# Performance work log

Measured on AMD Instinct MI355X. Metric: run time of the kernel, lower is better.

## Reference

```python
import jax, jax.numpy as jnp
import numpy as np

B, LD, LQ = 32, 512, 32
E, NF = 300, 4
D = E + NF            # doc_input_size = 304
M = 16                # fofe_max_length == max_len
ALPHA = 0.9
VOCAB = 50000
H = 256
SAMPLE_NUM = 256
POS_N = 128           # int(sample_num * (1 - neg_ratio))
NEG_N = SAMPLE_NUM - POS_N
R = min(M, LD - 2)    # candidate negative lengths = 16
PPL = NEG_N // R + 1  # negatives drawn per length = 9


def setup_inputs() -> dict:
    key = jax.random.key(0)
    ks = jax.random.split(key, 16)
    emb = jax.random.normal(ks[0], (VOCAB, E), jnp.float32) * 0.1
    emb = emb.at[0].set(0.0)  # padding_idx=0
    doc = jax.random.randint(ks[1], (B, LD), 1, VOCAB)
    doc_f = jax.random.normal(ks[2], (B, LD, NF), jnp.float32) * 0.1
    query = jax.random.randint(ks[3], (B, LQ), 1, VOCAB)
    target_s = jax.random.randint(ks[4], (B,), 1, LD - M - 2)
    span = jax.random.randint(ks[5], (B,), 0, M)  # ans_span = target_e - target_s < fofe_max_length
    target_e = target_s + span
    rand_length = jax.random.permutation(ks[6], R)  # torch.randperm(min(max_len, L-2))
    # rand_position[i] ~ randint(1, LD - rand_length[i] - 1)
    u = jax.random.uniform(ks[7], (R, PPL))
    size = (LD - rand_length - 2).astype(jnp.float32)[:, None]
    rand_position = 1 + jnp.floor(u * size).astype(jnp.int32)
    rand_idx = jax.random.randint(ks[8], (NEG_N,), 0, B)  # faithful to original (dim-0 size used as bound)
    perm_idx = jax.random.permutation(ks[9], SAMPLE_NUM)

    def w(k, o, i):
        return jax.random.normal(k, (o, i), jnp.float32) * (1.0 / np.sqrt(i))

    CIN = 3 * D + E  # 1212
    W1 = w(ks[10], 4 * H, CIN)
    W2 = w(ks[11], 4 * H, 4 * H)
    W3 = w(ks[12], 4 * H, 4 * H)
    W4 = w(ks[13], 2 * H, 4 * H)
    W5 = w(ks[14], 1, 2 * H)
    doc_mask = jnp.zeros((B, LD), bool)
    query_mask = jnp.zeros((B, LQ), bool)
    return dict(doc=doc, doc_f=doc_f, query=query, target_s=target_s, target_e=target_e,
                doc_mask=doc_mask, query_mask=query_mask, emb=emb,
                W1=W1, W2=W2, W3=W3, W4=W4, W5=W5,
                rand_length=rand_length, rand_position=rand_position,
                rand_idx=rand_idx, perm_idx=perm_idx)


def _fofe_codes(x):
    """x: [B, D, LD] -> forward/inverse FOFE codes [B, D, M, LD].
    fwd[b,c,l,t] = sum_{k=0}^{l} alpha^k x[b,c,t-k]; inv mirrors to the right."""
    fwd_terms = jnp.stack(
        [(ALPHA ** k) * jnp.pad(x, ((0, 0), (0, 0), (k, 0)))[..., :LD] for k in range(M)], axis=2)
    inv_terms = jnp.stack(
        [(ALPHA ** k) * jnp.pad(x, ((0, 0), (0, 0), (0, k)))[..., k:] for k in range(M)], axis=2)
    return jnp.cumsum(fwd_terms, axis=2), jnp.cumsum(inv_terms, axis=2)


def _cnn(x, W1, W2, W3, W4, W5):
    h = jax.nn.relu(jnp.einsum('oi,bis->bos', W1, x))
    h = jax.nn.relu(jnp.einsum('oi,bis->bos', W2, h))
    h = jax.nn.relu(jnp.einsum('oi,bis->bos', W3, h))
    h = jax.nn.relu(jnp.einsum('oi,bis->bos', W4, h))
    return jax.nn.sigmoid(jnp.einsum('oi,bis->bos', W5, h))


def reference(doc, doc_f, query, target_s, target_e, doc_mask, query_mask, emb,
              W1, W2, W3, W4, W5, rand_length, rand_position, rand_idx, perm_idx):
    # input_embedding (dropout_emb = 0, pos/ner disabled)
    doc_input = jnp.concatenate([emb[doc], doc_f], axis=-1)  # [B, LD, D]
    x = jnp.swapaxes(doc_input, 1, 2)                         # [B, D, LD]
    fwd, inv = _fofe_codes(x)                                 # [B, D, M, LD] each

    # --- positive samples: gold span + left/right full contexts ---
    b = jnp.arange(B)
    span = target_e - target_s
    ans = fwd[b, :, span, target_e]                               # [B, D]
    l_ctx = fwd[b, :, M - 1, jnp.maximum(target_s - 1, 0)]        # [B, D]
    r_ctx = inv[b, :, M - 1, jnp.minimum(target_e + 1, LD - 1)]   # [B, D]
    pos = jnp.concatenate([l_ctx, ans, r_ctx], axis=-1)          # [B, 3D]
    pos = jnp.broadcast_to(pos[:, :, None], (B, 3 * D, POS_N))

    # --- negative samples: random spans of each length in rand_length ---
    rl = rand_length[:, None]                                     # [R, 1]
    neg_ans = fwd[:, :, rl, rand_position].reshape(B, D, R * PPL)
    neg_l = fwd[:, :, M - 1, rand_position - 1].reshape(B, D, R * PPL)
    neg_r = inv[:, :, M - 1, rand_position + rl + 1].reshape(B, D, R * PPL)
    rand_cat = jnp.concatenate([neg_l, neg_ans, neg_r], axis=1)   # [B, 3D, R*PPL]
    neg = rand_cat[:, :, rand_idx]                                # [B, 3D, NEG_N]

    # --- shuffle pos+neg, build query FOFE, run cnn, mse (sum) loss ---
    ctx_ans = jnp.concatenate([pos, neg], axis=-1)[:, :, perm_idx]
    target = jnp.concatenate(
        [jnp.ones((B, 1, POS_N), jnp.float32), jnp.zeros((B, 1, NEG_N), jnp.float32)],
        axis=-1)[:, :, perm_idx]
    qw = ALPHA ** jnp.arange(LQ - 1, -1, -1, dtype=jnp.float32)   # fofe_linear weights
    qf = jnp.einsum('t,bte->be', qw, emb[query])                  # [B, E]
    qb = jnp.broadcast_to(qf[:, :, None], (B, E, SAMPLE_NUM))
    dq_input = jnp.concatenate([ctx_ans, qb], axis=1)             # [B, 3D+E, S]
    score = _cnn(dq_input, W1, W2, W3, W4, W5)                    # [B, 1, S]
    loss = jnp.sum((score - target) ** 2)                         # mse_loss(size_average=False)
    return loss
```

## Files before the change

kernel.cpp:

```cpp
#include <hip/hip_runtime.h>
#include <hip/hip_bf16.h>

#define B_    32
#define LD_   512
#define LQ_   32
#define E_    300
#define NF_   4
#define D_    304
#define M_    16
#define ALPHA_ 0.9f
#define CIN_  1212
#define KP1_  1280
#define NCOL_ 1056
#define NPAD_ 1088
#define PPL_  9
#define NEG_N_ 128

typedef short short8 __attribute__((ext_vector_type(8)));
typedef float f32x4 __attribute__((ext_vector_type(4)));

__device__ __forceinline__ unsigned short f2bf(float f) {
    unsigned int x = __float_as_uint(f);
    unsigned int r = (x + 0x7FFFu + ((x >> 16) & 1u)) >> 16;
    return (unsigned short)r;
}

__global__ __launch_bounds__(320) void prep(
    const int* __restrict__ doc, const float* __restrict__ doc_f,
    const int* __restrict__ query,
    const int* __restrict__ target_s, const int* __restrict__ target_e,
    const float* __restrict__ emb,
    const int* __restrict__ rand_length, const int* __restrict__ rand_position,
    const float* __restrict__ W1, const float* __restrict__ W2,
    const float* __restrict__ W3, const float* __restrict__ W4,
    unsigned short* __restrict__ W1b, unsigned short* __restrict__ W2b,
    unsigned short* __restrict__ W3b, unsigned short* __restrict__ W4b,
    unsigned short* __restrict__ Ft, float* __restrict__ zbuf,
    unsigned* __restrict__ done)
{
    int bid = blockIdx.x;
    int tid = threadIdx.x;

    if (bid < NCOL_) {
        int b = bid / 33;
        int col = bid % 33;
        __shared__ int   s_t[3][16];
        __shared__ float s_w[3][16];
        __shared__ int   s_row[3][16];
        if (tid < 48) {
            int part = tid >> 4, k = tid & 15;
            int t; float valid;
            if (col == 0) {
                int ts = target_s[b], te = target_e[b];
                int span = te - ts;
                if (part == 0)      { t = ts - 1 - k;  valid = (t >= 0) ? 1.f : 0.f; }
                else if (part == 1) { t = te - k;      valid = (k <= span && t >= 0) ? 1.f : 0.f; }
                else                { t = te + 1 + k;  valid = (t < LD_) ? 1.f : 0.f; }
            } else {
                int j = col - 1;
                int r = j / PPL_, p = j - r * PPL_;
                int rl = rand_length[r];
                int rp = rand_position[r * PPL_ + p];
                if (part == 0)      { t = rp - 1 - k;      valid = (t >= 0) ? 1.f : 0.f; }
                else if (part == 1) { t = rp - k;          valid = (k <= rl && t >= 0) ? 1.f : 0.f; }
                else                { t = rp + rl + 1 + k; valid = (t < LD_) ? 1.f : 0.f; }
            }
            float w = (valid != 0.f) ? powf(ALPHA_, (float)k) : 0.f;
            t = min(max(t, 0), LD_ - 1);
            s_t[part][k] = t;
            s_w[part][k] = w;
            s_row[part][k] = doc[b * LD_ + t];
        }
        __syncthreads();

        unsigned short* out = Ft + (size_t)bid * KP1_;
        int g = tid;
        if (g < 228) {
            int part = g / 76;
            int g2 = g - part * 76;
            int cc = g2 * 4;
            float ax = 0.f, ay = 0.f, az = 0.f, aw = 0.f;
            if (cc < 300) {
                for (int i = 0; i < 16; ++i) {
                    float4 v = *(const float4*)(emb + (size_t)s_row[part][i] * E_ + cc);
                    float wv = s_w[part][i];
                    ax += wv * v.x; ay += wv * v.y; az += wv * v.z; aw += wv * v.w;
                }
            } else {
                for (int i = 0; i < 16; ++i) {
                    float4 v = *(const float4*)(doc_f + ((size_t)b * LD_ + s_t[part][i]) * NF_);
                    float wv = s_w[part][i];
                    ax += wv * v.x; ay += wv * v.y; az += wv * v.z; aw += wv * v.w;
                }
            }
            ushort4 o; o.x = f2bf(ax); o.y = f2bf(ay); o.z = f2bf(az); o.w = f2bf(aw);
            *(ushort4*)(out + 4 * g) = o;
        } else if (g < 303) {
            int ce = (g - 228) * 4;
            float ax = 0.f, ay = 0.f, az = 0.f, aw = 0.f;
            float wv = powf(ALPHA_, (float)(LQ_ - 1));
            for (int i = 0; i < 32; ++i) {
                int row = query[b * LQ_ + i];
                float4 v = *(const float4*)(emb + (size_t)row * E_ + ce);
                ax += wv * v.x; ay += wv * v.y; az += wv * v.z; aw += wv * v.w;
                wv *= (1.0f / ALPHA_);
            }
            ushort4 o; o.x = f2bf(ax); o.y = f2bf(ay); o.z = f2bf(az); o.w = f2bf(aw);
            *(ushort4*)(out + 4 * g) = o;
        } else {
            ushort4 z; z.x = 0; z.y = 0; z.z = 0; z.w = 0;
            *(ushort4*)(out + 4 * g) = z;
        }
    } else if (bid < 2000) {
        const long n1 = 1024L * 320;
        const long n2 = 1024L * 1024L / 4;
        const long n4 = 512L * 1024L / 4;
        const long total = n1 + 2 * n2 + n4;
        long stride = 944L * 320L;
        for (long i = (long)(bid - NCOL_) * 320L + tid; i < total; i += stride) {
            ushort4 o;
            if (i < n1) {
                long m = i / 320; int k4 = (int)(i - m * 320);
                if (k4 < 303) {
                    float4 v = *(const float4*)(W1 + m * CIN_ + k4 * 4);
                    o.x = f2bf(v.x); o.y = f2bf(v.y); o.z = f2bf(v.z); o.w = f2bf(v.w);
                } else { o.x = 0; o.y = 0; o.z = 0; o.w = 0; }
                *(ushort4*)(W1b + i * 4) = o;
            } else if (i < n1 + n2) {
                long j = i - n1;
                float4 v = *(const float4*)(W2 + j * 4);
                o.x = f2bf(v.x); o.y = f2bf(v.y); o.z = f2bf(v.z); o.w = f2bf(v.w);
                *(ushort4*)(W2b + j * 4) = o;
            } else if (i < n1 + 2 * n2) {
                long j = i - n1 - n2;
                float4 v = *(const float4*)(W3 + j * 4);
                o.x = f2bf(v.x); o.y = f2bf(v.y); o.z = f2bf(v.z); o.w = f2bf(v.w);
                *(ushort4*)(W3b + j * 4) = o;
            } else {
                long j = i - n1 - 2 * n2;
                float4 v = *(const float4*)(W4 + j * 4);
                o.x = f2bf(v.x); o.y = f2bf(v.y); o.z = f2bf(v.z); o.w = f2bf(v.w);
                *(ushort4*)(W4b + j * 4) = o;
            }
        }
    } else if (bid < 2032) {
        int row = NCOL_ + (bid - 2000);
        ushort4 z; z.x = 0; z.y = 0; z.z = 0; z.w = 0;
        *(ushort4*)(Ft + (size_t)row * KP1_ + tid * 4) = z;
    } else {
        for (int i = tid; i < NPAD_; i += 320) zbuf[i] = 0.f;
        if (tid == 0) *done = 0u;
    }
}

struct GemmS { unsigned short A[2][64][72]; unsigned short B[2][64][72]; };

__device__ __forceinline__ void gemm_core(
    const unsigned short* __restrict__ A,
    const unsigned short* __restrict__ Bm,
    int K, int m0, int n0, GemmS& sh, f32x4 acc[4])
{
    int tid = threadIdx.x;
    int w = tid >> 6, lane = tid & 63;
    int wm = (w >> 1) * 32, wn = (w & 1) * 32;
    int lr = tid >> 2;
    int ls = (tid & 3) * 16;
    int fr = lane & 15, fk = (lane >> 4) * 8;

    const unsigned short* Arow = A + (size_t)(m0 + lr) * K + ls;
    const unsigned short* Brow = Bm + (size_t)(n0 + lr) * K + ls;

    #pragma unroll
    for (int t = 0; t < 4; ++t) { acc[t][0]=0.f; acc[t][1]=0.f; acc[t][2]=0.f; acc[t][3]=0.f; }

    int nk = K >> 6;
    *(uint4*)&sh.A[0][lr][ls]     = *(const uint4*)(Arow);
    *(uint4*)&sh.A[0][lr][ls + 8] = *(const uint4*)(Arow + 8);
    *(uint4*)&sh.B[0][lr][ls]     = *(const uint4*)(Brow);
    *(uint4*)&sh.B[0][lr][ls + 8] = *(const uint4*)(Brow + 8);
    __syncthreads();
    int cur = 0;
    for (int i = 0; i < nk; ++i) {
        uint4 na0, na1, nb0, nb1;
        bool more = (i + 1 < nk);
        if (more) {
            const unsigned short* An = Arow + (size_t)(i + 1) * 64;
            const unsigned short* Bn = Brow + (size_t)(i + 1) * 64;
            na0 = *(const uint4*)(An);
            na1 = *(const uint4*)(An + 8);
            nb0 = *(const uint4*)(Bn);
            nb1 = *(const uint4*)(Bn + 8);
        }
        #pragma unroll
        for (int s = 0; s < 2; ++s) {
            short8 fa0 = *(const short8*)&sh.A[cur][wm + fr][s * 32 + fk];
            short8 fa1 = *(const short8*)&sh.A[cur][wm + 16 + fr][s * 32 + fk];
            short8 fb0 = *(const short8*)&sh.B[cur][wn + fr][s * 32 + fk];
            short8 fb1 = *(const short8*)&sh.B[cur][wn + 16 + fr][s * 32 + fk];
            acc[0] = __builtin_amdgcn_mfma_f32_16x16x32_bf16(fa0, fb0, acc[0], 0, 0, 0);
            acc[1] = __builtin_amdgcn_mfma_f32_16x16x32_bf16(fa0, fb1, acc[1], 0, 0, 0);
            acc[2] = __builtin_amdgcn_mfma_f32_16x16x32_bf16(fa1, fb0, acc[2], 0, 0, 0);
            acc[3] = __builtin_amdgcn_mfma_f32_16x16x32_bf16(fa1, fb1, acc[3], 0, 0, 0);
        }
        if (more) {
            int nb = cur ^ 1;
            *(uint4*)&sh.A[nb][lr][ls]     = na0;
            *(uint4*)&sh.A[nb][lr][ls + 8] = na1;
            *(uint4*)&sh.B[nb][lr][ls]     = nb0;
            *(uint4*)&sh.B[nb][lr][ls + 8] = nb1;
        }
        __syncthreads();
        cur ^= 1;
    }
}

__global__ __launch_bounds__(256) void gemm_relu(
    const unsigned short* __restrict__ A,
    const unsigned short* __restrict__ Bm,
    unsigned short* __restrict__ C, int M, int K)
{
    __shared__ GemmS sh;
    int m0 = blockIdx.x * 64, n0 = blockIdx.y * 64;
    f32x4 acc[4];
    gemm_core(A, Bm, K, m0, n0, sh, acc);
    int tid = threadIdx.x;
    int w = tid >> 6, lane = tid & 63;
    int wm = (w >> 1) * 32, wn = (w & 1) * 32;
    int rbase = (lane >> 4) * 4;
    int cb = lane & 15;
    #pragma unroll
    for (int t = 0; t < 4; ++t) {
        int MT = t >> 1, NT = t & 1;
        int m = m0 + wm + MT * 16 + rbase;
        int n = n0 + wn + NT * 16 + cb;
        ushort4 o;
        o.x = f2bf(fmaxf(acc[t][0], 0.f));
        o.y = f2bf(fmaxf(acc[t][1], 0.f));
        o.z = f2bf(fmaxf(acc[t][2], 0.f));
        o.w = f2bf(fmaxf(acc[t][3], 0.f));
        *(ushort4*)(C + (size_t)n * M + m) = o;
    }
}

__global__ __launch_bounds__(256) void gemm4_score_loss(
    const unsigned short* __restrict__ A,
    const unsigned short* __restrict__ Bm,
    const float* __restrict__ W5, const int* __restrict__ rand_idx,
    float* __restrict__ zbuf, unsigned* __restrict__ done,
    float* __restrict__ out, int M, int K)
{
    __shared__ GemmS sh;
    __shared__ int s_flag;
    __shared__ int s_cnt[32];
    __shared__ float s_red[256];
    int m0 = blockIdx.x * 64, n0 = blockIdx.y * 64;
    f32x4 acc[4];
    gemm_core(A, Bm, K, m0, n0, sh, acc);
    int tid = threadIdx.x;
    int w = tid >> 6, lane = tid & 63;
    int wm = (w >> 1) * 32, wn = (w & 1) * 32;
    int fr = lane & 15, fq = lane >> 4;
    #pragma unroll
    for (int NT = 0; NT < 2; ++NT) {
        float p = 0.f;
        #pragma unroll
        for (int MT = 0; MT < 2; ++MT) {
            const f32x4 a = acc[MT * 2 + NT];
            int mb = m0 + wm + MT * 16 + fq * 4;
            p += fmaxf(a[0], 0.f) * W5[mb]
               + fmaxf(a[1], 0.f) * W5[mb + 1]
               + fmaxf(a[2], 0.f) * W5[mb + 2]
               + fmaxf(a[3], 0.f) * W5[mb + 3];
        }
        p += __shfl_down(p, 32);
        p += __shfl_down(p, 16);
        if (fq == 0) {
            int n = n0 + wn + NT * 16 + fr;
            atomicAdd(&zbuf[n], p);
        }
    }
    __syncthreads();
    if (tid == 0) {
        unsigned old = __hip_atomic_fetch_add(done, 1u, __ATOMIC_ACQ_REL,
                                              __HIP_MEMORY_SCOPE_AGENT);
        s_flag = (old == 8 * 17 - 1) ? 1 : 0;
    }
    __syncthreads();
    if (s_flag) {
        if (tid < 32) s_cnt[tid] = 0;
        __syncthreads();
        if (tid < NEG_N_) atomicAdd(&s_cnt[rand_idx[tid]], 1);
        __syncthreads();
        float accv = 0.f;
        for (int c = tid; c < NCOL_; c += 256) {
            float z = __hip_atomic_load(&zbuf[c], __ATOMIC_ACQUIRE,
                                        __HIP_MEMORY_SCOPE_AGENT);
            float s = 1.f / (1.f + expf(-z));
            int c33 = c % 33;
            if (c33 == 0) { float d = s - 1.f; accv += 128.f * d * d; }
            else          { accv += (float)s_cnt[c33 - 1] * s * s; }
        }
        s_red[tid] = accv;
        __syncthreads();
        for (int o = 128; o > 0; o >>= 1) {
            if (tid < o) s_red[tid] += s_red[tid + o];
            __syncthreads();
        }
        if (tid == 0) out[0] = s_red[0];
    }
}

extern "C" void kernel_launch(void* const* d_in, const int* in_sizes, int n_in,
                              void* d_out, int out_size, void* d_ws, size_t ws_size,
                              hipStream_t stream)
{
    const int*   doc        = (const int*)d_in[0];
    const float* doc_f      = (const float*)d_in[1];
    const int*   query      = (const int*)d_in[2];
    const int*   target_s   = (const int*)d_in[3];
    const int*   target_e   = (const int*)d_in[4];
    const float* emb        = (const float*)d_in[7];
    const float* W1         = (const float*)d_in[8];
    const float* W2         = (const float*)d_in[9];
    const float* W3         = (const float*)d_in[10];
    const float* W4         = (const float*)d_in[11];
    const float* W5         = (const float*)d_in[12];
    const int*   rand_length   = (const int*)d_in[13];
    const int*   rand_position = (const int*)d_in[14];
    const int*   rand_idx      = (const int*)d_in[15];

    char* ws = (char*)d_ws;
    size_t off = 0;
    auto alloc = [&](size_t bytes) {
        void* p = ws + off;
        off = (off + bytes + 255) & ~(size_t)255;
        return p;
    };
    unsigned short* W1b = (unsigned short*)alloc((size_t)1024 * KP1_ * 2);
    unsigned short* W2b = (unsigned short*)alloc((size_t)1024 * 1024 * 2);
    unsigned short* W3b = (unsigned short*)alloc((size_t)1024 * 1024 * 2);
    unsigned short* W4b = (unsigned short*)alloc((size_t)512 * 1024 * 2);
    unsigned short* Ft  = (unsigned short*)alloc((size_t)NPAD_ * KP1_ * 2);
    unsigned short* hA  = (unsigned short*)alloc((size_t)NPAD_ * 1024 * 2);
    unsigned short* hB  = (unsigned short*)alloc((size_t)NPAD_ * 1024 * 2);
    float*    zbuf      = (float*)alloc((size_t)NPAD_ * sizeof(float));
    unsigned* done      = (unsigned*)alloc(256);
    (void)ws_size; (void)in_sizes; (void)n_in; (void)out_size;

    prep<<<dim3(2033), dim3(320), 0, stream>>>(
        doc, doc_f, query, target_s, target_e, emb,
        rand_length, rand_position,
        W1, W2, W3, W4, W1b, W2b, W3b, W4b, Ft, zbuf, done);

    gemm_relu<<<dim3(16, 17), dim3(256), 0, stream>>>(W1b, Ft, hA, 1024, KP1_);
    gemm_relu<<<dim3(16, 17), dim3(256), 0, stream>>>(W2b, hA, hB, 1024, 1024);
    gemm_relu<<<dim3(16, 17), dim3(256), 0, stream>>>(W3b, hB, hA, 1024, 1024);
    gemm4_score_loss<<<dim3(8, 17), dim3(256), 0, stream>>>(
        W4b, hA, W5, rand_idx, zbuf, done, (float*)d_out, 512, 1024);
}
```

Baseline: 189.1 us.

## Shrink GEMM tiles to raise block count and trim first-layer K padding

The MLP GEMMs move from 64x64 tiles to 32x64 tiles, and the final score GEMM moves to 32x32 tiles. This roughly doubles or quadruples the number of workgroups so more of the many compute units stay busy on these small matrices. The first-layer reduction dimension is cut from 1280 to 1216, which removes padded K iterations. The powf calls are replaced by a constant table of alpha powers. Each block now does less reuse per tile and the grid launches more blocks, so there are more global loads per flop and more atomics into the score buffer.

Result: no change. 190.4 us (+0.6%).

```diff
diff --git a/kernel.cpp b/kernel.cpp
--- a/kernel.cpp
+++ b/kernel.cpp
@@ -10,7 +10,7 @@
 #define M_    16
 #define ALPHA_ 0.9f
 #define CIN_  1212
-#define KP1_  1280
+#define KP1_  1216
 #define NCOL_ 1056
 #define NPAD_ 1088
 #define PPL_  9
@@ -18,6 +18,18 @@
 
 typedef short short8 __attribute__((ext_vector_type(8)));
 typedef float f32x4 __attribute__((ext_vector_type(4)));
+
+__device__ __constant__ float A_POW[32] = {
+    1.0f, 0.9f, 0.81f, 0.729f, 0.6561f, 0.59049f, 0.531441f, 0.4782969f,
+    0.43046721f, 0.387420489f, 0.3486784401f, 0.31381059609f,
+    0.282429536481f, 0.2541865828329f, 0.22876792454961f, 0.205891132094649f,
+    0.18530201888518416f, 0.16677181699666577f, 0.1500946352969992f,
+    0.13508517176729928f, 0.12157665459056935f, 0.10941898913151242f,
+    0.09847709021836118f, 0.08862938119652507f, 0.07976644307687256f,
+    0.0717897987691853f, 0.06461081889226677f, 0.05814973700304009f,
+    0.05233476330273608f, 0.047101286972462474f, 0.042391158275216226f,
+    0.038152042447694604f
+};
 
 __device__ __forceinline__ unsigned short f2bf(float f) {
     unsigned int x = __float_as_uint(f);
@@ -65,7 +77,7 @@
                 else if (part == 1) { t = rp - k;          valid = (k <= rl && t >= 0) ? 1.f : 0.f; }
                 else                { t = rp + rl + 1 + k; valid = (t < LD_) ? 1.f : 0.f; }
             }
-            float w = (valid != 0.f) ? powf(ALPHA_, (float)k) : 0.f;
+            float w = (valid != 0.f) ? A_POW[k] : 0.f;
             t = min(max(t, 0), LD_ - 1);
             s_t[part][k] = t;
             s_w[part][k] = w;
@@ -98,21 +110,20 @@
         } else if (g < 303) {
             int ce = (g - 228) * 4;
             float ax = 0.f, ay = 0.f, az = 0.f, aw = 0.f;
-            float wv = powf(ALPHA_, (float)(LQ_ - 1));
             for (int i = 0; i < 32; ++i) {
                 int row = query[b * LQ_ + i];
+                float wv = A_POW[LQ_ - 1 - i];
                 float4 v = *(const float4*)(emb + (size_t)row * E_ + ce);
                 ax += wv * v.x; ay += wv * v.y; az += wv * v.z; aw += wv * v.w;
-                wv *= (1.0f / ALPHA_);
             }
             ushort4 o; o.x = f2bf(ax); o.y = f2bf(ay); o.z = f2bf(az); o.w = f2bf(aw);
             *(ushort4*)(out + 4 * g) = o;
-        } else {
+        } else if (g == 303) {
             ushort4 z; z.x = 0; z.y = 0; z.z = 0; z.w = 0;
             *(ushort4*)(out + 4 * g) = z;
         }
     } else if (bid < 2000) {
-        const long n1 = 1024L * 320;
+        const long n1 = 1024L * 304;
         const long n2 = 1024L * 1024L / 4;
         const long n4 = 512L * 1024L / 4;
         const long total = n1 + 2 * n2 + n4;
@@ -120,7 +131,7 @@
         for (long i = (long)(bid - NCOL_) * 320L + tid; i < total; i += stride) {
             ushort4 o;
             if (i < n1) {
-                long m = i / 320; int k4 = (int)(i - m * 320);
+                long m = i / 304; int k4 = (int)(i - m * 304);
                 if (k4 < 303) {
                     float4 v = *(const float4*)(W1 + m * CIN_ + k4 * 4);
                     o.x = f2bf(v.x); o.y = f2bf(v.y); o.z = f2bf(v.z); o.w = f2bf(v.w);
@@ -145,69 +156,65 @@
         }
     } else if (bid < 2032) {
         int row = NCOL_ + (bid - 2000);
-        ushort4 z; z.x = 0; z.y = 0; z.z = 0; z.w = 0;
-        *(ushort4*)(Ft + (size_t)row * KP1_ + tid * 4) = z;
+        if (tid < 304) {
+            ushort4 z; z.x = 0; z.y = 0; z.z = 0; z.w = 0;
+            *(ushort4*)(Ft + (size_t)row * KP1_ + tid * 4) = z;
+        }
     } else {
         for (int i = tid; i < NPAD_; i += 320) zbuf[i] = 0.f;
         if (tid == 0) *done = 0u;
     }
 }
 
-struct GemmS { unsigned short A[2][64][72]; unsigned short B[2][64][72]; };
-
-__device__ __forceinline__ void gemm_core(
+struct GemmS64 { unsigned short A[2][32][72]; unsigned short B[2][64][72]; };
+
+__device__ __forceinline__ void gemm_core_3264(
     const unsigned short* __restrict__ A,
     const unsigned short* __restrict__ Bm,
-    int K, int m0, int n0, GemmS& sh, f32x4 acc[4])
+    int K, int m0, int n0, GemmS64& sh, f32x4 acc[2])
 {
     int tid = threadIdx.x;
     int w = tid >> 6, lane = tid & 63;
-    int wm = (w >> 1) * 32, wn = (w & 1) * 32;
-    int lr = tid >> 2;
-    int ls = (tid & 3) * 16;
+    int wm = (w & 1) * 16, wn = (w >> 1) * 32;
     int fr = lane & 15, fk = (lane >> 4) * 8;
-
-    const unsigned short* Arow = A + (size_t)(m0 + lr) * K + ls;
-    const unsigned short* Brow = Bm + (size_t)(n0 + lr) * K + ls;
-
-    #pragma unroll
-    for (int t = 0; t < 4; ++t) { acc[t][0]=0.f; acc[t][1]=0.f; acc[t][2]=0.f; acc[t][3]=0.f; }
+    int arow = tid >> 3, acol = (tid & 7) * 8;
+    int brow = tid >> 2, bcol = (tid & 3) * 16;
+
+    const unsigned short* Ap = A + (size_t)(m0 + arow) * K + acol;
+    const unsigned short* Bp = Bm + (size_t)(n0 + brow) * K + bcol;
+
+    acc[0][0]=0.f; acc[0][1]=0.f; acc[0][2]=0.f; acc[0][3]=0.f;
+    acc[1][0]=0.f; acc[1][1]=0.f; acc[1][2]=0.f; acc[1][3]=0.f;
 
     int nk = K >> 6;
-    *(uint4*)&sh.A[0][lr][ls]     = *(const uint4*)(Arow);
-    *(uint4*)&sh.A[0][lr][ls + 8] = *(const uint4*)(Arow + 8);
-    *(uint4*)&sh.B[0][lr][ls]     = *(const uint4*)(Brow);
-    *(uint4*)&sh.B[0][lr][ls + 8] = *(const uint4*)(Brow + 8);
+    *(uint4*)&sh.A[0][arow][acol]     = *(const uint4*)(Ap);
+    *(uint4*)&sh.B[0][brow][bcol]     = *(const uint4*)(Bp);
+    *(uint4*)&sh.B[0][brow][bcol + 8] = *(const uint4*)(Bp + 8);
     __syncthreads();
     int cur = 0;
     for (int i = 0; i < nk; ++i) {
-        uint4 na0, na1, nb0, nb1;
+        uint4 na, nb0, nb1;
         bool more = (i + 1 < nk);
         if (more) {
-            const unsigned short* An = Arow + (size_t)(i + 1) * 64;
-            const unsigned short* Bn = Brow + (size_t)(i + 1) * 64;
-            na0 = *(const uint4*)(An);
-            na1 = *(const uint4*)(An + 8);
+            const unsigned short* An = Ap + (size_t)(i + 1) * 64;
+            const unsigned short* Bn = Bp + (size_t)(i + 1) * 64;
+            na  = *(const uint4*)(An);
             nb0 = *(const uint4*)(Bn);
             nb1 = *(const uint4*)(Bn + 8);
         }
         #pragma unroll
         for (int s = 0; s < 2; ++s) {
-            short8 fa0 = *(const short8*)&sh.A[cur][wm + fr][s * 32 + fk];
-            short8 fa1 = *(const short8*)&sh.A[cur][wm + 16 + fr][s * 32 + fk];
+            short8 fa = *(const short8*)&sh.A[cur][wm + fr][s * 32 + fk];
             short8 fb0 = *(const short8*)&sh.B[cur][wn + fr][s * 32 + fk];
             short8 fb1 = *(const short8*)&sh.B[cur][wn + 16 + fr][s * 32 + fk];
-            acc[0] = __builtin_amdgcn_mfma_f32_16x16x32_bf16(fa0, fb0, acc[0], 0, 0, 0);
-            acc[1] = __builtin_amdgcn_mfma_f32_16x16x32_bf16(fa0, fb1, acc[1], 0, 0, 0);
-            acc[2] = __builtin_amdgcn_mfma_f32_16x16x32_bf16(fa1, fb0, acc[2], 0, 0, 0);
-            acc[3] = __builtin_amdgcn_mfma_f32_16x16x32_bf16(fa1, fb1, acc[3], 0, 0, 0);
+            acc[0] = __builtin_amdgcn_mfma_f32_16x16x32_bf16(fa, fb0, acc[0], 0, 0, 0);
+            acc[1] = __builtin_amdgcn_mfma_f32_16x16x32_bf16(fa, fb1, acc[1], 0, 0, 0);
         }
         if (more) {
             int nb = cur ^ 1;
-            *(uint4*)&sh.A[nb][lr][ls]     = na0;
-            *(uint4*)&sh.A[nb][lr][ls + 8] = na1;
-            *(uint4*)&sh.B[nb][lr][ls]     = nb0;
-            *(uint4*)&sh.B[nb][lr][ls + 8] = nb1;
+            *(uint4*)&sh.A[nb][arow][acol]     = na;
+            *(uint4*)&sh.B[nb][brow][bcol]     = nb0;
+            *(uint4*)&sh.B[nb][brow][bcol + 8] = nb1;
         }
         __syncthreads();
         cur ^= 1;
@@ -219,28 +226,29 @@
     const unsigned short* __restrict__ Bm,
     unsigned short* __restrict__ C, int M, int K)
 {
-    __shared__ GemmS sh;
-    int m0 = blockIdx.x * 64, n0 = blockIdx.y * 64;
-    f32x4 acc[4];
-    gemm_core(A, Bm, K, m0, n0, sh, acc);
+    __shared__ GemmS64 sh;
+    int m0 = blockIdx.x * 32, n0 = blockIdx.y * 64;
+    f32x4 acc[2];
+    gemm_core_3264(A, Bm, K, m0, n0, sh, acc);
     int tid = threadIdx.x;
     int w = tid >> 6, lane = tid & 63;
-    int wm = (w >> 1) * 32, wn = (w & 1) * 32;
+    int wm = (w & 1) * 16, wn = (w >> 1) * 32;
     int rbase = (lane >> 4) * 4;
     int cb = lane & 15;
     #pragma unroll
-    for (int t = 0; t < 4; ++t) {
-        int MT = t >> 1, NT = t & 1;
-        int m = m0 + wm + MT * 16 + rbase;
-        int n = n0 + wn + NT * 16 + cb;
+    for (int nt = 0; nt < 2; ++nt) {
+        int m = m0 + wm + rbase;
+        int n = n0 + wn + nt * 16 + cb;
         ushort4 o;
-        o.x = f2bf(fmaxf(acc[t][0], 0.f));
-        o.y = f2bf(fmaxf(acc[t][1], 0.f));
-        o.z = f2bf(fmaxf(acc[t][2], 0.f));
-        o.w = f2bf(fmaxf(acc[t][3], 0.f));
+        o.x = f2bf(fmaxf(acc[nt][0], 0.f));
+        o.y = f2bf(fmaxf(acc[nt][1], 0.f));
+        o.z = f2bf(fmaxf(acc[nt][2], 0.f));
+        o.w = f2bf(fmaxf(acc[nt][3], 0.f));
         *(ushort4*)(C + (size_t)n * M + m) = o;
     }
 }
+
+struct GemmS32 { unsigned short A[2][32][72]; unsigned short B[2][32][72]; };
 
 __global__ __launch_bounds__(256) void gemm4_score_loss(
     const unsigned short* __restrict__ A,
@@ -249,41 +257,67 @@
     float* __restrict__ zbuf, unsigned* __restrict__ done,
     float* __restrict__ out, int M, int K)
 {
-    __shared__ GemmS sh;
+    __shared__ GemmS32 sh;
     __shared__ int s_flag;
     __shared__ int s_cnt[32];
     __shared__ float s_red[256];
-    int m0 = blockIdx.x * 64, n0 = blockIdx.y * 64;
-    f32x4 acc[4];
-    gemm_core(A, Bm, K, m0, n0, sh, acc);
     int tid = threadIdx.x;
     int w = tid >> 6, lane = tid & 63;
-    int wm = (w >> 1) * 32, wn = (w & 1) * 32;
-    int fr = lane & 15, fq = lane >> 4;
-    #pragma unroll
-    for (int NT = 0; NT < 2; ++NT) {
-        float p = 0.f;
+    int wm = (w & 1) * 16, wn = (w >> 1) * 16;
+    int fr = lane & 15, fq = lane >> 4, fk = fq * 8;
+    int arow = tid >> 3, acol = (tid & 7) * 8;
+    int m0 = blockIdx.x * 32, n0 = blockIdx.y * 32;
+
+    const unsigned short* Ap = A + (size_t)(m0 + arow) * K + acol;
+    const unsigned short* Bp = Bm + (size_t)(n0 + arow) * K + acol;
+
+    f32x4 acc = {0.f, 0.f, 0.f, 0.f};
+    int nk = K >> 6;
+    *(uint4*)&sh.A[0][arow][acol] = *(const uint4*)(Ap);
+    *(uint4*)&sh.B[0][arow][acol] = *(const uint4*)(Bp);
+    __syncthreads();
+    int cur = 0;
+    for (int i = 0; i < nk; ++i) {
+        uint4 na, nb;
+        bool more = (i + 1 < nk);
+        if (more) {
+            na = *(const uint4*)(Ap + (size_t)(i + 1) * 64);
+            nb = *(const uint4*)(Bp + (size_t)(i + 1) * 64);
+        }
         #pragma unroll
-        for (int MT = 0; MT < 2; ++MT) {
-            const f32x4 a = acc[MT * 2 + NT];
-            int mb = m0 + wm + MT * 16 + fq * 4;
-            p += fmaxf(a[0], 0.f) * W5[mb]
-               + fmaxf(a[1], 0.f) * W5[mb + 1]
-               + fmaxf(a[2], 0.f) * W5[mb + 2]
-               + fmaxf(a[3], 0.f) * W5[mb + 3];
-        }
+        for (int s = 0; s < 2; ++s) {
+            short8 fa = *(const short8*)&sh.A[cur][wm + fr][s * 32 + fk];
+            short8 fb = *(const short8*)&sh.B[cur][wn + fr][s * 32 + fk];
+            acc = __builtin_amdgcn_mfma_f32_16x16x32_bf16(fa, fb, acc, 0, 0, 0);
+        }
+        if (more) {
+            int nb2 = cur ^ 1;
+            *(uint4*)&sh.A[nb2][arow][acol] = na;
+            *(uint4*)&sh.B[nb2][arow][acol] = nb;
+        }
+        __syncthreads();
+        cur ^= 1;
+    }
+
+    {
+        int mb = m0 + wm + fq * 4;
+        float p = fmaxf(acc[0], 0.f) * W5[mb]
+                + fmaxf(acc[1], 0.f) * W5[mb + 1]
+                + fmaxf(acc[2], 0.f) * W5[mb + 2]
+                + fmaxf(acc[3], 0.f) * W5[mb + 3];
         p += __shfl_down(p, 32);
         p += __shfl_down(p, 16);
         if (fq == 0) {
-            int n = n0 + wn + NT * 16 + fr;
+            int n = n0 + wn + fr;
             atomicAdd(&zbuf[n], p);
         }
     }
     __syncthreads();
     if (tid == 0) {
+        unsigned total = gridDim.x * gridDim.y;
         unsigned old = __hip_atomic_fetch_add(done, 1u, __ATOMIC_ACQ_REL,
                                               __HIP_MEMORY_SCOPE_AGENT);
-        s_flag = (old == 8 * 17 - 1) ? 1 : 0;
+        s_flag = (old == total - 1) ? 1 : 0;
     }
     __syncthreads();
     if (s_flag) {
@@ -352,9 +386,9 @@
         rand_length, rand_position,
         W1, W2, W3, W4, W1b, W2b, W3b, W4b, Ft, zbuf, done);
 
-    gemm_relu<<<dim3(16, 17), dim3(256), 0, stream>>>(W1b, Ft, hA, 1024, KP1_);
-    gemm_relu<<<dim3(16, 17), dim3(256), 0, stream>>>(W2b, hA, hB, 1024, 1024);
-    gemm_relu<<<dim3(16, 17), dim3(256), 0, stream>>>(W3b, hB, hA, 1024, 1024);
-    gemm4_score_loss<<<dim3(8, 17), dim3(256), 0, stream>>>(
+    gemm_relu<<<dim3(32, 17), dim3(256), 0, stream>>>(W1b, Ft, hA, 1024, KP1_);
+    gemm_relu<<<dim3(32, 17), dim3(256), 0, stream>>>(W2b, hA, hB, 1024, 1024);
+    gemm_relu<<<dim3(32, 17), dim3(256), 0, stream>>>(W3b, hB, hA, 1024, 1024);
+    gemm4_score_loss<<<dim3(16, 34), dim3(256), 0, stream>>>(
         W4b, hA, W5, rand_idx, zbuf, done, (float*)d_out, 512, 1024);
 }
```

## Deepen GEMM register prefetch, trim layer-1 K padding, tabulate alpha powers

Applied to the files above, without the earlier changes.

The GEMM mainloop now prefetches global tiles two K-steps ahead into a pair of register slots instead of one step ahead. The goal is to hide more global-load latency behind the MFMA work. The first-layer K padding shrinks from 1280 to 1216, which is still a multiple of 64, so the layer-1 GEMM runs one fewer K-iteration and the prep kernel writes less padding. Runtime powf calls are replaced by a constant table of alpha powers. The risks are that runtime-indexed register arrays may spill to scratch and that keeping more values live raises register pressure.

Measured after the change: 286.8 us. +51.6%, slower.

```diff
diff --git a/kernel.cpp b/kernel.cpp
--- a/kernel.cpp
+++ b/kernel.cpp
@@ -10,7 +10,7 @@
 #define M_    16
 #define ALPHA_ 0.9f
 #define CIN_  1212
-#define KP1_  1280
+#define KP1_  1216
 #define NCOL_ 1056
 #define NPAD_ 1088
 #define PPL_  9
@@ -18,6 +18,18 @@
 
 typedef short short8 __attribute__((ext_vector_type(8)));
 typedef float f32x4 __attribute__((ext_vector_type(4)));
+
+__device__ __constant__ float A_POW[32] = {
+    1.0f, 0.9f, 0.81f, 0.729f, 0.6561f, 0.59049f, 0.531441f, 0.4782969f,
+    0.43046721f, 0.387420489f, 0.3486784401f, 0.31381059609f,
+    0.282429536481f, 0.2541865828329f, 0.22876792454961f, 0.205891132094649f,
+    0.18530201888518416f, 0.16677181699666577f, 0.1500946352969992f,
+    0.13508517176729928f, 0.12157665459056935f, 0.10941898913151242f,
+    0.09847709021836118f, 0.08862938119652507f, 0.07976644307687256f,
+    0.0717897987691853f, 0.06461081889226677f, 0.05814973700304009f,
+    0.05233476330273608f, 0.047101286972462474f, 0.042391158275216226f,
+    0.038152042447694604f
+};
 
 __device__ __forceinline__ unsigned short f2bf(float f) {
     unsigned int x = __float_as_uint(f);
@@ -65,7 +77,7 @@
                 else if (part == 1) { t = rp - k;          valid = (k <= rl && t >= 0) ? 1.f : 0.f; }
                 else                { t = rp + rl + 1 + k; valid = (t < LD_) ? 1.f : 0.f; }
             }
-            float w = (valid != 0.f) ? powf(ALPHA_, (float)k) : 0.f;
+            float w = (valid != 0.f) ? A_POW[k] : 0.f;
             t = min(max(t, 0), LD_ - 1);
             s_t[part][k] = t;
             s_w[part][k] = w;
@@ -98,21 +110,20 @@
         } else if (g < 303) {
             int ce = (g - 228) * 4;
             float ax = 0.f, ay = 0.f, az = 0.f, aw = 0.f;
-            float wv = powf(ALPHA_, (float)(LQ_ - 1));
             for (int i = 0; i < 32; ++i) {
                 int row = query[b * LQ_ + i];
+                float wv = A_POW[LQ_ - 1 - i];
                 float4 v = *(const float4*)(emb + (size_t)row * E_ + ce);
                 ax += wv * v.x; ay += wv * v.y; az += wv * v.z; aw += wv * v.w;
-                wv *= (1.0f / ALPHA_);
             }
             ushort4 o; o.x = f2bf(ax); o.y = f2bf(ay); o.z = f2bf(az); o.w = f2bf(aw);
             *(ushort4*)(out + 4 * g) = o;
-        } else {
+        } else if (g == 303) {
             ushort4 z; z.x = 0; z.y = 0; z.z = 0; z.w = 0;
             *(ushort4*)(out + 4 * g) = z;
         }
     } else if (bid < 2000) {
-        const long n1 = 1024L * 320;
+        const long n1 = 1024L * 304;
         const long n2 = 1024L * 1024L / 4;
         const long n4 = 512L * 1024L / 4;
         const long total = n1 + 2 * n2 + n4;
@@ -120,7 +131,7 @@
         for (long i = (long)(bid - NCOL_) * 320L + tid; i < total; i += stride) {
             ushort4 o;
             if (i < n1) {
-                long m = i / 320; int k4 = (int)(i - m * 320);
+                long m = i / 304; int k4 = (int)(i - m * 304);
                 if (k4 < 303) {
                     float4 v = *(const float4*)(W1 + m * CIN_ + k4 * 4);
                     o.x = f2bf(v.x); o.y = f2bf(v.y); o.z = f2bf(v.z); o.w = f2bf(v.w);
@@ -145,8 +156,10 @@
         }
     } else if (bid < 2032) {
         int row = NCOL_ + (bid - 2000);
-        ushort4 z; z.x = 0; z.y = 0; z.z = 0; z.w = 0;
-        *(ushort4*)(Ft + (size_t)row * KP1_ + tid * 4) = z;
+        if (tid < 304) {
+            ushort4 z; z.x = 0; z.y = 0; z.z = 0; z.w = 0;
+            *(ushort4*)(Ft + (size_t)row * KP1_ + tid * 4) = z;
+        }
     } else {
         for (int i = tid; i < NPAD_; i += 320) zbuf[i] = 0.f;
         if (tid == 0) *done = 0u;
@@ -174,22 +187,26 @@
     for (int t = 0; t < 4; ++t) { acc[t][0]=0.f; acc[t][1]=0.f; acc[t][2]=0.f; acc[t][3]=0.f; }
 
     int nk = K >> 6;
-    *(uint4*)&sh.A[0][lr][ls]     = *(const uint4*)(Arow);
-    *(uint4*)&sh.A[0][lr][ls + 8] = *(const uint4*)(Arow + 8);
-    *(uint4*)&sh.B[0][lr][ls]     = *(const uint4*)(Brow);
-    *(uint4*)&sh.B[0][lr][ls + 8] = *(const uint4*)(Brow + 8);
+    uint4 ra0[2], ra1[2], rb0[2], rb1[2];
+    ra0[0] = *(const uint4*)(Arow);      ra1[0] = *(const uint4*)(Arow + 8);
+    rb0[0] = *(const uint4*)(Brow);      rb1[0] = *(const uint4*)(Brow + 8);
+    ra0[1] = *(const uint4*)(Arow + 64); ra1[1] = *(const uint4*)(Arow + 72);
+    rb0[1] = *(const uint4*)(Brow + 64); rb1[1] = *(const uint4*)(Brow + 72);
+    *(uint4*)&sh.A[0][lr][ls]     = ra0[0];
+    *(uint4*)&sh.A[0][lr][ls + 8] = ra1[0];
+    *(uint4*)&sh.B[0][lr][ls]     = rb0[0];
+    *(uint4*)&sh.B[0][lr][ls + 8] = rb1[0];
     __syncthreads();
     int cur = 0;
     for (int i = 0; i < nk; ++i) {
-        uint4 na0, na1, nb0, nb1;
-        bool more = (i + 1 < nk);
-        if (more) {
-            const unsigned short* An = Arow + (size_t)(i + 1) * 64;
-            const unsigned short* Bn = Brow + (size_t)(i + 1) * 64;
-            na0 = *(const uint4*)(An);
-            na1 = *(const uint4*)(An + 8);
-            nb0 = *(const uint4*)(Bn);
-            nb1 = *(const uint4*)(Bn + 8);
+        int sl = i & 1;
+        if (i + 2 < nk) {
+            const unsigned short* An = Arow + (size_t)(i + 2) * 64;
+            const unsigned short* Bn = Brow + (size_t)(i + 2) * 64;
+            ra0[sl] = *(const uint4*)(An);
+            ra1[sl] = *(const uint4*)(An + 8);
+            rb0[sl] = *(const uint4*)(Bn);
+            rb1[sl] = *(const uint4*)(Bn + 8);
         }
         #pragma unroll
         for (int s = 0; s < 2; ++s) {
@@ -202,12 +219,12 @@
             acc[2] = __builtin_amdgcn_mfma_f32_16x16x32_bf16(fa1, fb0, acc[2], 0, 0, 0);
             acc[3] = __builtin_amdgcn_mfma_f32_16x16x32_bf16(fa1, fb1, acc[3], 0, 0, 0);
         }
-        if (more) {
-            int nb = cur ^ 1;
-            *(uint4*)&sh.A[nb][lr][ls]     = na0;
-            *(uint4*)&sh.A[nb][lr][ls + 8] = na1;
-            *(uint4*)&sh.B[nb][lr][ls]     = nb0;
-            *(uint4*)&sh.B[nb][lr][ls + 8] = nb1;
+        if (i + 1 < nk) {
+            int ns = (i + 1) & 1, nb = cur ^ 1;
+            *(uint4*)&sh.A[nb][lr][ls]     = ra0[ns];
+            *(uint4*)&sh.A[nb][lr][ls + 8] = ra1[ns];
+            *(uint4*)&sh.B[nb][lr][ls]     = rb0[ns];
+            *(uint4*)&sh.B[nb][lr][ls + 8] = rb1[ns];
         }
         __syncthreads();
         cur ^= 1;
```
